# Performance work log

Measured on AMD Instinct MI355X. Metric: run time of the kernel, lower is better.

Reference implementation:

```python
import jax, jax.numpy as jnp
import numpy as np

N = 50000      # nodes
E = 200000     # edges
IN = 768       # in_dim
HID = 256      # hidden_dim
OUT = 64       # out_dim
H = 4          # heads in conv1
R = 6          # n_relations
NEG = 0.2      # LeakyReLU negative slope (PyG default)
EPS = 1e-5     # LayerNorm eps


def layer_norm(h, g, b):
    mu = jnp.mean(h, axis=-1, keepdims=True)
    var = jnp.mean((h - mu) ** 2, axis=-1, keepdims=True)
    return (h - mu) * jax.lax.rsqrt(var + EPS) * g + b


def gat_layer(x, src, dst, W, a_src, a_dst, bias, heads, dh):
    # project: [N, heads, dh]
    h = (x @ W).reshape(-1, heads, dh)
    # per-node attention logits [N, heads]
    al_s = jnp.sum(h * a_src, axis=-1)
    al_d = jnp.sum(h * a_dst, axis=-1)
    # per-edge scores (edge j->i: source contributes al_s[j], target al_d[i])
    e = jax.nn.leaky_relu(al_s[src] + al_d[dst], NEG)  # [E, heads]
    # segment softmax over edges sharing the same destination node
    e_max = jax.ops.segment_max(e, dst, num_segments=N)        # [N, heads]
    ex = jnp.exp(e - e_max[dst])                               # [E, heads]
    denom = jax.ops.segment_sum(ex, dst, num_segments=N)       # [N, heads]
    alpha = ex / denom[dst]                                    # [E, heads]
    # weighted scatter-aggregate of source messages
    msg = h[src] * alpha[:, :, None]                            # [E, heads, dh]
    out = jax.ops.segment_sum(msg, dst, num_segments=N)        # [N, heads, dh]
    return out.reshape(-1, heads * dh) + bias


def setup_inputs() -> dict:
    key = jax.random.key(0)
    ks = jax.random.split(key, 16)
    s = 0.05  # keep attention logits tame
    return {
        "x": jax.random.normal(ks[0], (N, IN), jnp.float32),
        "edge_index": jax.random.randint(ks[1], (2, E), 0, N, dtype=jnp.int64),
        "edge_type": jax.random.randint(ks[2], (E,), 0, R, dtype=jnp.int64),
        "edge_emb": jax.random.normal(ks[3], (R, IN), jnp.float32) * s,
        "W1": jax.random.normal(ks[4], (IN, H * (HID // H)), jnp.float32) * s,
        "a_src1": jax.random.normal(ks[5], (H, HID // H), jnp.float32) * s,
        "a_dst1": jax.random.normal(ks[6], (H, HID // H), jnp.float32) * s,
        "b1": jnp.zeros((HID,), jnp.float32),
        "g1": jnp.ones((HID,), jnp.float32),
        "be1": jnp.zeros((HID,), jnp.float32),
        "W2": jax.random.normal(ks[7], (HID, OUT), jnp.float32) * s,
        "a_src2": jax.random.normal(ks[8], (1, OUT), jnp.float32) * s,
        "a_dst2": jax.random.normal(ks[9], (1, OUT), jnp.float32) * s,
        "b2": jnp.zeros((OUT,), jnp.float32),
        "g2": jnp.ones((OUT,), jnp.float32),
        "be2": jnp.zeros((OUT,), jnp.float32),
    }


def reference(x, edge_index, edge_type, edge_emb, W1, a_src1, a_dst1, b1, g1, be1,
              W2, a_src2, a_dst2, b2, g2, be2):
    src, dst = edge_index[0], edge_index[1]
    edge_feat = edge_emb[edge_type]                 # [E, IN]
    x_mod = x.at[src].set(x[src] + edge_feat)
    h = gat_layer(x_mod, src, dst, W1, a_src1, a_dst1, b1, H, HID // H)
    h = layer_norm(h, g1, be1)
    h = jax.nn.elu(h)                                # dropout off (inference)
    h = gat_layer(h, src, dst, W2, a_src2, a_dst2, b2, 1, OUT)
    h = layer_norm(h, g2, be2)
    return h
```

## Files before the change

### kernel.cpp

```cpp
#include <hip/hip_runtime.h>
#include <cstdint>
#include <cstddef>

#define NN 50000
#define NE 200000
#define IND 768
#define HID 256
#define OUTD 64
#define NB 196

typedef __bf16 bf16;
typedef __bf16 bf16x8 __attribute__((ext_vector_type(8)));
typedef float f32x4 __attribute__((ext_vector_type(4)));

__global__ __launch_bounds__(256) void k_scatter_last(const int* __restrict__ ei,
                                                      int* __restrict__ le) {
  int e = blockIdx.x * 256 + threadIdx.x;
  if (e < NE) atomicMax(&le[ei[e]], e);
}

__global__ __launch_bounds__(256) void k_xmod(const float* __restrict__ x,
                                              const int* __restrict__ le,
                                              const int* __restrict__ etype,
                                              const float* __restrict__ eemb,
                                              bf16* __restrict__ xmod) {
  int row = blockIdx.y;
  int col = blockIdx.x * 256 + threadIdx.x;
  int l = le[row];
  float v = x[(size_t)row * IND + col];
  if (l >= 0) v += eemb[etype[l] * IND + col];
  xmod[(size_t)row * IND + col] = (bf16)v;
}

__global__ __launch_bounds__(256) void k_hist(const int* __restrict__ ei, int* __restrict__ deg) {
  int e = blockIdx.x * 256 + threadIdx.x;
  if (e < NE) atomicAdd(&deg[ei[NE + e]], 1);
}

__global__ __launch_bounds__(256) void k_scan_block(const int* __restrict__ deg,
                                                    int* __restrict__ excl, int* __restrict__ bsum) {
  __shared__ int sm[256];
  int tid = threadIdx.x;
  int i = blockIdx.x * 256 + tid;
  int v = (i < NN) ? deg[i] : 0;
  sm[tid] = v;
  __syncthreads();
#pragma unroll
  for (int off = 1; off < 256; off <<= 1) {
    int t = (tid >= off) ? sm[tid - off] : 0;
    __syncthreads();
    sm[tid] += t;
    __syncthreads();
  }
  if (i < NN) excl[i] = sm[tid] - v;
  if (tid == 255) bsum[blockIdx.x] = sm[255];
}

__global__ __launch_bounds__(256) void k_scan_partials(const int* __restrict__ bsum,
                                                       int* __restrict__ bbase) {
  __shared__ int sm[256];
  int tid = threadIdx.x;
  int v = (tid < NB) ? bsum[tid] : 0;
  sm[tid] = v;
  __syncthreads();
#pragma unroll
  for (int off = 1; off < 256; off <<= 1) {
    int t = (tid >= off) ? sm[tid - off] : 0;
    __syncthreads();
    sm[tid] += t;
    __syncthreads();
  }
  bbase[tid] = sm[tid] - v;
}

__global__ __launch_bounds__(256) void k_add_base(const int* __restrict__ excl,
                                                  const int* __restrict__ bbase,
                                                  int* __restrict__ rowstart, int* __restrict__ cur) {
  int i = blockIdx.x * 256 + threadIdx.x;
  if (i < NN) {
    int rs = excl[i] + bbase[i >> 8];
    rowstart[i] = rs;
    cur[i] = rs;
  }
}

__global__ __launch_bounds__(256) void k_scatter_csr(const int* __restrict__ ei,
                                                     int* __restrict__ cur, int* __restrict__ csr) {
  int e = blockIdx.x * 256 + threadIdx.x;
  if (e < NE) {
    int d = ei[NE + e];
    int pos = atomicAdd(&cur[d], 1);
    csr[pos] = ei[e];
  }
}

__global__ __launch_bounds__(256) void k_transpose(const float* __restrict__ W,
                                                   bf16* __restrict__ Wt, int K, int NC) {
  int k = blockIdx.x * 256 + threadIdx.x;
  int n = blockIdx.y;
  if (k < K) Wt[n * K + k] = (bf16)W[k * NC + n];
}

template <typename OutT>
__global__ __launch_bounds__(256) void k_gemm_bt(const bf16* __restrict__ A,
                                                 const bf16* __restrict__ Bt,
                                                 OutT* __restrict__ C,
                                                 int M, int K, int NC) {
  __shared__ bf16 As[128 * 32];
  __shared__ bf16 Bs[128 * 32];
  const int tid = threadIdx.x;
  const int lane = tid & 63;
  const int wave = tid >> 6;
  const int wr = wave >> 1, wc = wave & 1;
  const int ln15 = lane & 15, q = lane >> 4;
  const int m0 = blockIdx.x * 128;
  const int n0 = blockIdx.y * 128;
  const int r0 = tid >> 2;
  const int ce = (tid & 3) << 3;

  f32x4 acc[4][4] = {};

  for (int kt = 0; kt < K; kt += 32) {
    int ra1 = min(m0 + r0, M - 1) * K + kt + ce;
    int ra2 = min(m0 + 64 + r0, M - 1) * K + kt + ce;
    int rb1 = min(n0 + r0, NC - 1) * K + kt + ce;
    int rb2 = min(n0 + 64 + r0, NC - 1) * K + kt + ce;
    int4 va1 = *(const int4*)(A + ra1);
    int4 va2 = *(const int4*)(A + ra2);
    int4 vb1 = *(const int4*)(Bt + rb1);
    int4 vb2 = *(const int4*)(Bt + rb2);
    __syncthreads();
    *(int4*)(As + r0 * 32 + ce) = va1;
    *(int4*)(As + (64 + r0) * 32 + ce) = va2;
    *(int4*)(Bs + r0 * 32 + ce) = vb1;
    *(int4*)(Bs + (64 + r0) * 32 + ce) = vb2;
    __syncthreads();
    bf16x8 af[4], bfr[4];
#pragma unroll
    for (int i = 0; i < 4; i++)
      af[i] = *(const bf16x8*)(As + (wr * 64 + i * 16 + ln15) * 32 + q * 8);
#pragma unroll
    for (int i = 0; i < 4; i++)
      bfr[i] = *(const bf16x8*)(Bs + (wc * 64 + i * 16 + ln15) * 32 + q * 8);
#pragma unroll
    for (int mi = 0; mi < 4; mi++)
#pragma unroll
      for (int ni = 0; ni < 4; ni++)
        acc[mi][ni] = __builtin_amdgcn_mfma_f32_16x16x32_bf16(af[mi], bfr[ni], acc[mi][ni], 0, 0, 0);
  }
#pragma unroll
  for (int mi = 0; mi < 4; mi++)
#pragma unroll
    for (int ni = 0; ni < 4; ni++)
#pragma unroll
      for (int r = 0; r < 4; r++) {
        int row = m0 + wr * 64 + mi * 16 + q * 4 + r;
        int col = n0 + wc * 64 + ni * 16 + ln15;
        if (row < M && col < NC) C[(size_t)row * NC + col] = (OutT)acc[mi][ni][r];
      }
}

__global__ __launch_bounds__(256) void k_al1(const bf16* __restrict__ h1,
                                             const float* __restrict__ aS,
                                             const float* __restrict__ aD,
                                             float* __restrict__ alS, float* __restrict__ alD) {
  int n = blockIdx.x, f = threadIdx.x;
  float hv = (float)h1[(size_t)n * HID + f];
  float s1 = hv * aS[f], s2 = hv * aD[f];
#pragma unroll
  for (int off = 32; off; off >>= 1) { s1 += __shfl_xor(s1, off); s2 += __shfl_xor(s2, off); }
  if ((f & 63) == 0) { alS[n * 4 + (f >> 6)] = s1; alD[n * 4 + (f >> 6)] = s2; }
}

__global__ __launch_bounds__(256) void k_agg_ln1(const int* __restrict__ rowstart,
                                                 const int* __restrict__ deg,
                                                 const int* __restrict__ csr,
                                                 const bf16* __restrict__ h1,
                                                 const float* __restrict__ alS,
                                                 const float* __restrict__ alD,
                                                 const float* __restrict__ b1,
                                                 const float* __restrict__ g1,
                                                 const float* __restrict__ be1,
                                                 bf16* __restrict__ hln) {
  __shared__ float red[8];
  int n = blockIdx.x, f = threadIdx.x, hd = f >> 6;
  int start = rowstart[n], cnt = deg[n];
  float ald = alD[n * 4 + hd];
  float accv = 0.f, accw = 0.f;
  for (int j = 0; j < cnt; j++) {
    int s = csr[start + j];
    float logit = alS[s * 4 + hd] + ald;
    logit = logit >= 0.f ? logit : 0.2f * logit;
    float w = __expf(logit);
    accv += w * (float)h1[(size_t)s * HID + f];
    accw += w;
  }
  float v = (cnt > 0) ? accv / accw : 0.f;
  v += b1[f];
  float s = v, ss = v * v;
#pragma unroll
  for (int off = 32; off; off >>= 1) { s += __shfl_xor(s, off); ss += __shfl_xor(ss, off); }
  if ((f & 63) == 0) { red[f >> 6] = s; red[4 + (f >> 6)] = ss; }
  __syncthreads();
  float tot = red[0] + red[1] + red[2] + red[3];
  float tss = red[4] + red[5] + red[6] + red[7];
  float mu = tot * (1.f / HID);
  float var = tss * (1.f / HID) - mu * mu;
  float y = (v - mu) * rsqrtf(var + 1e-5f) * g1[f] + be1[f];
  y = y > 0.f ? y : __expf(y) - 1.f;
  hln[(size_t)n * HID + f] = (bf16)y;
}

__global__ __launch_bounds__(256) void k_al2(const float* __restrict__ h2,
                                             const float* __restrict__ aS,
                                             const float* __restrict__ aD,
                                             float* __restrict__ alS, float* __restrict__ alD) {
  int n = blockIdx.x * 4 + (threadIdx.x >> 6);
  int f = threadIdx.x & 63;
  float hv = h2[(size_t)n * OUTD + f];
  float s1 = hv * aS[f], s2 = hv * aD[f];
#pragma unroll
  for (int off = 32; off; off >>= 1) { s1 += __shfl_xor(s1, off); s2 += __shfl_xor(s2, off); }
  if (f == 0) { alS[n] = s1; alD[n] = s2; }
}

__global__ __launch_bounds__(64) void k_agg_ln2(const int* __restrict__ rowstart,
                                                const int* __restrict__ deg,
                                                const int* __restrict__ csr,
                                                const float* __restrict__ h2,
                                                const float* __restrict__ alS,
                                                const float* __restrict__ alD,
                                                const float* __restrict__ b2,
                                                const float* __restrict__ g2,
                                                const float* __restrict__ be2,
                                                float* __restrict__ out) {
  int n = blockIdx.x, f = threadIdx.x;
  int start = rowstart[n], cnt = deg[n];
  float ald = alD[n];
  float accv = 0.f, accw = 0.f;
  for (int j = 0; j < cnt; j++) {
    int s = csr[start + j];
    float logit = alS[s] + ald;
    logit = logit >= 0.f ? logit : 0.2f * logit;
    float w = __expf(logit);
    accv += w * h2[(size_t)s * OUTD + f];
    accw += w;
  }
  float v = (cnt > 0) ? accv / accw : 0.f;
  v += b2[f];
  float s = v, ss = v * v;
#pragma unroll
  for (int off = 32; off; off >>= 1) { s += __shfl_xor(s, off); ss += __shfl_xor(ss, off); }
  float mu = s * (1.f / OUTD);
  float var = ss * (1.f / OUTD) - mu * mu;
  out[(size_t)n * OUTD + f] = (v - mu) * rsqrtf(var + 1e-5f) * g2[f] + be2[f];
}

extern "C" void kernel_launch(void* const* d_in, const int* in_sizes, int n_in,
                              void* d_out, int out_size, void* d_ws, size_t ws_size,
                              hipStream_t stream) {
  const float* x    = (const float*)d_in[0];
  const int*   ei   = (const int*)d_in[1];
  const int*   et   = (const int*)d_in[2];
  const float* eemb = (const float*)d_in[3];
  const float* W1   = (const float*)d_in[4];
  const float* as1  = (const float*)d_in[5];
  const float* ad1  = (const float*)d_in[6];
  const float* b1   = (const float*)d_in[7];
  const float* g1   = (const float*)d_in[8];
  const float* be1  = (const float*)d_in[9];
  const float* W2   = (const float*)d_in[10];
  const float* as2  = (const float*)d_in[11];
  const float* ad2  = (const float*)d_in[12];
  const float* b2   = (const float*)d_in[13];
  const float* g2   = (const float*)d_in[14];
  const float* be2  = (const float*)d_in[15];
  float* out = (float*)d_out;

  char* base = (char*)d_ws;
  size_t off = 0;
  auto alloc = [&](size_t bytes) -> void* {
    void* p = base + off;
    off = (off + bytes + 255) & ~(size_t)255;
    return p;
  };
  int*   le    = (int*)alloc((size_t)NN * 4);
  int*   deg   = (int*)alloc((size_t)NN * 4);
  int*   excl  = (int*)alloc((size_t)NN * 4);
  int*   bsum  = (int*)alloc(256 * 4);
  int*   bbase = (int*)alloc(256 * 4);
  int*   rowst = (int*)alloc((size_t)NN * 4);
  int*   cur   = (int*)alloc((size_t)NN * 4);
  int*   csr   = (int*)alloc((size_t)NE * 4);
  bf16*  h1    = (bf16*)alloc((size_t)NN * HID * 2);
  float* alS1  = (float*)alloc((size_t)NN * 4 * 4);
  float* alD1  = (float*)alloc((size_t)NN * 4 * 4);
  bf16*  hln   = (bf16*)alloc((size_t)NN * HID * 2);
  float* h2    = (float*)alloc((size_t)NN * OUTD * 4);
  float* alS2  = (float*)alloc((size_t)NN * 4);
  float* alD2  = (float*)alloc((size_t)NN * 4);
  bf16*  W1t   = (bf16*)alloc((size_t)HID * IND * 2);
  bf16*  W2t   = (bf16*)alloc((size_t)OUTD * HID * 2);
  bf16*  xmod  = (bf16*)alloc((size_t)NN * IND * 2);

  hipMemsetAsync(le, 0xFF, (size_t)NN * 4, stream);
  hipMemsetAsync(deg, 0, (size_t)NN * 4, stream);

  k_scatter_last<<<(NE + 255) / 256, 256, 0, stream>>>(ei, le);
  k_hist<<<(NE + 255) / 256, 256, 0, stream>>>(ei, deg);
  k_scan_block<<<NB, 256, 0, stream>>>(deg, excl, bsum);
  k_scan_partials<<<1, 256, 0, stream>>>(bsum, bbase);
  k_add_base<<<NB, 256, 0, stream>>>(excl, bbase, rowst, cur);
  k_scatter_csr<<<(NE + 255) / 256, 256, 0, stream>>>(ei, cur, csr);

  k_transpose<<<dim3(3, HID), 256, 0, stream>>>(W1, W1t, IND, HID);
  k_transpose<<<dim3(1, OUTD), 256, 0, stream>>>(W2, W2t, HID, OUTD);
  k_xmod<<<dim3(3, NN), 256, 0, stream>>>(x, le, et, eemb, xmod);

  k_gemm_bt<bf16><<<dim3((NN + 127) / 128, 2), 256, 0, stream>>>(xmod, W1t, h1, NN, IND, HID);
  k_al1<<<NN, 256, 0, stream>>>(h1, as1, ad1, alS1, alD1);
  k_agg_ln1<<<NN, 256, 0, stream>>>(rowst, deg, csr, h1, alS1, alD1, b1, g1, be1, hln);

  k_gemm_bt<float><<<dim3((NN + 127) / 128, 1), 256, 0, stream>>>(hln, W2t, h2, NN, HID, OUTD);
  k_al2<<<NN / 4, 256, 0, stream>>>(h2, as2, ad2, alS2, alD2);
  k_agg_ln2<<<NN, 64, 0, stream>>>(rowst, deg, csr, h2, alS2, alD2, b2, g2, be2, out);
}
```

Measured before the change: 534.2 us.

## Fuse x_mod construction and attention logits into GEMM, merge edge prep kernels

```diff
diff --git a/kernel.cpp b/kernel.cpp
--- a/kernel.cpp
+++ b/kernel.cpp
@@ -13,28 +13,13 @@
 typedef __bf16 bf16x8 __attribute__((ext_vector_type(8)));
 typedef float f32x4 __attribute__((ext_vector_type(4)));
 
-__global__ __launch_bounds__(256) void k_scatter_last(const int* __restrict__ ei,
-                                                      int* __restrict__ le) {
+__global__ __launch_bounds__(256) void k_edge_prep(const int* __restrict__ ei,
+                                                   int* __restrict__ le, int* __restrict__ deg) {
   int e = blockIdx.x * 256 + threadIdx.x;
-  if (e < NE) atomicMax(&le[ei[e]], e);
-}
-
-__global__ __launch_bounds__(256) void k_xmod(const float* __restrict__ x,
-                                              const int* __restrict__ le,
-                                              const int* __restrict__ etype,
-                                              const float* __restrict__ eemb,
-                                              bf16* __restrict__ xmod) {
-  int row = blockIdx.y;
-  int col = blockIdx.x * 256 + threadIdx.x;
-  int l = le[row];
-  float v = x[(size_t)row * IND + col];
-  if (l >= 0) v += eemb[etype[l] * IND + col];
-  xmod[(size_t)row * IND + col] = (bf16)v;
-}
-
-__global__ __launch_bounds__(256) void k_hist(const int* __restrict__ ei, int* __restrict__ deg) {
-  int e = blockIdx.x * 256 + threadIdx.x;
-  if (e < NE) atomicAdd(&deg[ei[NE + e]], 1);
+  if (e < NE) {
+    atomicMax(&le[ei[e]], e);
+    atomicAdd(&deg[ei[NE + e]], 1);
+  }
 }
 
 __global__ __launch_bounds__(256) void k_scan_block(const int* __restrict__ deg,
@@ -101,11 +86,20 @@
   if (k < K) Wt[n * K + k] = (bf16)W[k * NC + n];
 }
 
-template <typename OutT>
+template <typename OutT, bool FUSE>
 __global__ __launch_bounds__(256) void k_gemm_bt(const bf16* __restrict__ A,
+                                                 const float* __restrict__ Ax,
+                                                 const int* __restrict__ le,
+                                                 const int* __restrict__ et,
+                                                 const float* __restrict__ eemb,
                                                  const bf16* __restrict__ Bt,
                                                  OutT* __restrict__ C,
-                                                 int M, int K, int NC) {
+                                                 int M, int K, int NC,
+                                                 const float* __restrict__ aS,
+                                                 const float* __restrict__ aD,
+                                                 float* __restrict__ alS,
+                                                 float* __restrict__ alD,
+                                                 int alStride) {
   __shared__ bf16 As[128 * 32];
   __shared__ bf16 Bs[128 * 32];
   const int tid = threadIdx.x;
@@ -113,27 +107,64 @@
   const int wave = tid >> 6;
   const int wr = wave >> 1, wc = wave & 1;
   const int ln15 = lane & 15, q = lane >> 4;
-  const int m0 = blockIdx.x * 128;
-  const int n0 = blockIdx.y * 128;
+  const int n0 = blockIdx.x * 128;
+  const int m0 = blockIdx.y * 128;
   const int r0 = tid >> 2;
   const int ce = (tid & 3) << 3;
 
+  const int rA1 = min(m0 + r0, M - 1);
+  const int rA2 = min(m0 + 64 + r0, M - 1);
+  const int rB1 = min(n0 + r0, NC - 1);
+  const int rB2 = min(n0 + 64 + r0, NC - 1);
+
+  int e1 = -1, e2 = -1;
+  if (FUSE) {
+    int l1 = le[rA1]; if (l1 >= 0) e1 = et[l1];
+    int l2 = le[rA2]; if (l2 >= 0) e2 = et[l2];
+  }
+
   f32x4 acc[4][4] = {};
 
   for (int kt = 0; kt < K; kt += 32) {
-    int ra1 = min(m0 + r0, M - 1) * K + kt + ce;
-    int ra2 = min(m0 + 64 + r0, M - 1) * K + kt + ce;
-    int rb1 = min(n0 + r0, NC - 1) * K + kt + ce;
-    int rb2 = min(n0 + 64 + r0, NC - 1) * K + kt + ce;
-    int4 va1 = *(const int4*)(A + ra1);
-    int4 va2 = *(const int4*)(A + ra2);
-    int4 vb1 = *(const int4*)(Bt + rb1);
-    int4 vb2 = *(const int4*)(Bt + rb2);
-    __syncthreads();
-    *(int4*)(As + r0 * 32 + ce) = va1;
-    *(int4*)(As + (64 + r0) * 32 + ce) = va2;
-    *(int4*)(Bs + r0 * 32 + ce) = vb1;
-    *(int4*)(Bs + (64 + r0) * 32 + ce) = vb2;
+    bf16x8 va, vb;
+    int4 va_i, vb_i;
+    if (FUSE) {
+      const float* p1 = Ax + (size_t)rA1 * K + kt + ce;
+      const float* p2 = Ax + (size_t)rA2 * K + kt + ce;
+      float4 a0 = *(const float4*)p1, a1 = *(const float4*)(p1 + 4);
+      float4 b0 = *(const float4*)p2, b1 = *(const float4*)(p2 + 4);
+      if (e1 >= 0) {
+        const float* q1 = eemb + (size_t)e1 * K + kt + ce;
+        float4 t0 = *(const float4*)q1, t1 = *(const float4*)(q1 + 4);
+        a0.x += t0.x; a0.y += t0.y; a0.z += t0.z; a0.w += t0.w;
+        a1.x += t1.x; a1.y += t1.y; a1.z += t1.z; a1.w += t1.w;
+      }
+      if (e2 >= 0) {
+        const float* q2 = eemb + (size_t)e2 * K + kt + ce;
+        float4 t0 = *(const float4*)q2, t1 = *(const float4*)(q2 + 4);
+        b0.x += t0.x; b0.y += t0.y; b0.z += t0.z; b0.w += t0.w;
+        b1.x += t1.x; b1.y += t1.y; b1.z += t1.z; b1.w += t1.w;
+      }
+      va[0] = (bf16)a0.x; va[1] = (bf16)a0.y; va[2] = (bf16)a0.z; va[3] = (bf16)a0.w;
+      va[4] = (bf16)a1.x; va[5] = (bf16)a1.y; va[6] = (bf16)a1.z; va[7] = (bf16)a1.w;
+      vb[0] = (bf16)b0.x; vb[1] = (bf16)b0.y; vb[2] = (bf16)b0.z; vb[3] = (bf16)b0.w;
+      vb[4] = (bf16)b1.x; vb[5] = (bf16)b1.y; vb[6] = (bf16)b1.z; vb[7] = (bf16)b1.w;
+    } else {
+      va_i = *(const int4*)(A + (size_t)rA1 * K + kt + ce);
+      vb_i = *(const int4*)(A + (size_t)rA2 * K + kt + ce);
+    }
+    int4 wb1 = *(const int4*)(Bt + (size_t)rB1 * K + kt + ce);
+    int4 wb2 = *(const int4*)(Bt + (size_t)rB2 * K + kt + ce);
+    __syncthreads();
+    if (FUSE) {
+      *(bf16x8*)(As + r0 * 32 + ce) = va;
+      *(bf16x8*)(As + (64 + r0) * 32 + ce) = vb;
+    } else {
+      *(int4*)(As + r0 * 32 + ce) = va_i;
+      *(int4*)(As + (64 + r0) * 32 + ce) = vb_i;
+    }
+    *(int4*)(Bs + r0 * 32 + ce) = wb1;
+    *(int4*)(Bs + (64 + r0) * 32 + ce) = wb2;
     __syncthreads();
     bf16x8 af[4], bfr[4];
 #pragma unroll
@@ -148,6 +179,7 @@
       for (int ni = 0; ni < 4; ni++)
         acc[mi][ni] = __builtin_amdgcn_mfma_f32_16x16x32_bf16(af[mi], bfr[ni], acc[mi][ni], 0, 0, 0);
   }
+
 #pragma unroll
   for (int mi = 0; mi < 4; mi++)
 #pragma unroll
@@ -158,18 +190,34 @@
         int col = n0 + wc * 64 + ni * 16 + ln15;
         if (row < M && col < NC) C[(size_t)row * NC + col] = (OutT)acc[mi][ni][r];
       }
-}
-
-__global__ __launch_bounds__(256) void k_al1(const bf16* __restrict__ h1,
-                                             const float* __restrict__ aS,
-                                             const float* __restrict__ aD,
-                                             float* __restrict__ alS, float* __restrict__ alD) {
-  int n = blockIdx.x, f = threadIdx.x;
-  float hv = (float)h1[(size_t)n * HID + f];
-  float s1 = hv * aS[f], s2 = hv * aD[f];
-#pragma unroll
-  for (int off = 32; off; off >>= 1) { s1 += __shfl_xor(s1, off); s2 += __shfl_xor(s2, off); }
-  if ((f & 63) == 0) { alS[n * 4 + (f >> 6)] = s1; alD[n * 4 + (f >> 6)] = s2; }
+
+  if (n0 + wc * 64 < NC) {
+    const int hd = (n0 + wc * 64) >> 6;
+#pragma unroll
+    for (int mi = 0; mi < 4; mi++)
+#pragma unroll
+      for (int r = 0; r < 4; r++) {
+        float ps = 0.f, pd = 0.f;
+#pragma unroll
+        for (int ni = 0; ni < 4; ni++) {
+          int col = n0 + wc * 64 + ni * 16 + ln15;
+          float w_s = (col < NC) ? aS[col] : 0.f;
+          float w_d = (col < NC) ? aD[col] : 0.f;
+          ps += acc[mi][ni][r] * w_s;
+          pd += acc[mi][ni][r] * w_d;
+        }
+#pragma unroll
+        for (int off = 1; off < 16; off <<= 1) {
+          ps += __shfl_xor(ps, off);
+          pd += __shfl_xor(pd, off);
+        }
+        int row = m0 + wr * 64 + mi * 16 + q * 4 + r;
+        if (ln15 == 0 && row < M) {
+          alS[row * alStride + hd] = ps;
+          alD[row * alStride + hd] = pd;
+        }
+      }
+  }
 }
 
 __global__ __launch_bounds__(256) void k_agg_ln1(const int* __restrict__ rowstart,
@@ -209,19 +257,6 @@
   float y = (v - mu) * rsqrtf(var + 1e-5f) * g1[f] + be1[f];
   y = y > 0.f ? y : __expf(y) - 1.f;
   hln[(size_t)n * HID + f] = (bf16)y;
-}
-
-__global__ __launch_bounds__(256) void k_al2(const float* __restrict__ h2,
-                                             const float* __restrict__ aS,
-                                             const float* __restrict__ aD,
-                                             float* __restrict__ alS, float* __restrict__ alD) {
-  int n = blockIdx.x * 4 + (threadIdx.x >> 6);
-  int f = threadIdx.x & 63;
-  float hv = h2[(size_t)n * OUTD + f];
-  float s1 = hv * aS[f], s2 = hv * aD[f];
-#pragma unroll
-  for (int off = 32; off; off >>= 1) { s1 += __shfl_xor(s1, off); s2 += __shfl_xor(s2, off); }
-  if (f == 0) { alS[n] = s1; alD[n] = s2; }
 }
 
 __global__ __launch_bounds__(64) void k_agg_ln2(const int* __restrict__ rowstart,
@@ -301,13 +336,11 @@
   float* alD2  = (float*)alloc((size_t)NN * 4);
   bf16*  W1t   = (bf16*)alloc((size_t)HID * IND * 2);
   bf16*  W2t   = (bf16*)alloc((size_t)OUTD * HID * 2);
-  bf16*  xmod  = (bf16*)alloc((size_t)NN * IND * 2);
 
   hipMemsetAsync(le, 0xFF, (size_t)NN * 4, stream);
   hipMemsetAsync(deg, 0, (size_t)NN * 4, stream);
 
-  k_scatter_last<<<(NE + 255) / 256, 256, 0, stream>>>(ei, le);
-  k_hist<<<(NE + 255) / 256, 256, 0, stream>>>(ei, deg);
+  k_edge_prep<<<(NE + 255) / 256, 256, 0, stream>>>(ei, le, deg);
   k_scan_block<<<NB, 256, 0, stream>>>(deg, excl, bsum);
   k_scan_partials<<<1, 256, 0, stream>>>(bsum, bbase);
   k_add_base<<<NB, 256, 0, stream>>>(excl, bbase, rowst, cur);
@@ -315,13 +348,12 @@
 
   k_transpose<<<dim3(3, HID), 256, 0, stream>>>(W1, W1t, IND, HID);
   k_transpose<<<dim3(1, OUTD), 256, 0, stream>>>(W2, W2t, HID, OUTD);
-  k_xmod<<<dim3(3, NN), 256, 0, stream>>>(x, le, et, eemb, xmod);
-
-  k_gemm_bt<bf16><<<dim3((NN + 127) / 128, 2), 256, 0, stream>>>(xmod, W1t, h1, NN, IND, HID);
-  k_al1<<<NN, 256, 0, stream>>>(h1, as1, ad1, alS1, alD1);
+
+  k_gemm_bt<bf16, true><<<dim3(2, (NN + 127) / 128), 256, 0, stream>>>(
+      nullptr, x, le, et, eemb, W1t, h1, NN, IND, HID, as1, ad1, alS1, alD1, 4);
   k_agg_ln1<<<NN, 256, 0, stream>>>(rowst, deg, csr, h1, alS1, alD1, b1, g1, be1, hln);
 
-  k_gemm_bt<float><<<dim3((NN + 127) / 128, 1), 256, 0, stream>>>(hln, W2t, h2, NN, HID, OUTD);
-  k_al2<<<NN / 4, 256, 0, stream>>>(h2, as2, ad2, alS2, alD2);
+  k_gemm_bt<float, false><<<dim3(1, (NN + 127) / 128), 256, 0, stream>>>(
+      hln, nullptr, nullptr, nullptr, nullptr, W2t, h2, NN, HID, OUTD, as2, ad2, alS2, alD2, 1);
   k_agg_ln2<<<NN, 64, 0, stream>>>(rowst, deg, csr, h2, alS2, alD2, b2, g2, be2, out);
 }
```

Result: faster. 480.0 us (-10.1%).
